# Kernel tuning notes

Hardware: AMD Instinct MI355X
Metric: run time of the kernel (lower is better)

## Reference

```python
import jax, jax.numpy as jnp
import numpy as np

D_INNER = 5120
DT_RANK = 160
N_STATE = 16
BATCH = 256


def _softplus_thresh20(x):
    # ttnn.softplus(parameter1=1.0, parameter2=20.0): linear above threshold 20
    return jnp.where(x > 20.0, x, jnp.log1p(jnp.exp(jnp.minimum(x, 20.0))))


def setup_inputs() -> dict:
    key = jax.random.key(0)
    ks = jax.random.split(key, 9)
    x = jax.random.normal(ks[0], (1, 1, BATCH, D_INNER), dtype=jnp.float32)
    # scale weights by 1/sqrt(fan_in) so softplus input is O(1)
    W_dt_low = jax.random.normal(ks[1], (D_INNER, DT_RANK), dtype=jnp.float32) / np.sqrt(D_INNER)
    W_dt = jax.random.normal(ks[2], (DT_RANK, D_INNER), dtype=jnp.float32) / np.sqrt(DT_RANK)
    b_dt = jax.random.normal(ks[3], (D_INNER,), dtype=jnp.float32)
    W_B = jax.random.normal(ks[4], (D_INNER, N_STATE), dtype=jnp.float32) / np.sqrt(D_INNER)
    W_C = jax.random.normal(ks[5], (D_INNER, N_STATE), dtype=jnp.float32) / np.sqrt(D_INNER)
    # A = -exp(A_log): strictly negative, as in the module's preprocess_A
    A = -jnp.exp(0.5 * jax.random.normal(ks[6], (D_INNER, N_STATE), dtype=jnp.float32))
    D = jax.random.normal(ks[7], (D_INNER,), dtype=jnp.float32)
    h0 = 0.1 * jax.random.normal(ks[8], (BATCH, D_INNER, N_STATE), dtype=jnp.float32)
    return {"x": x, "W_dt_low": W_dt_low, "W_dt": W_dt, "b_dt": b_dt,
            "W_B": W_B, "W_C": W_C, "A": A, "D": D, "h0": h0}


def reference(x, W_dt_low, W_dt, b_dt, W_B, W_C, A, D, h0):
    b, d = x.shape[2], x.shape[3]
    xb = x.reshape(b, d)                                  # (B, D)
    # delta = softplus(x @ x_proj_dt @ dt_proj + bias)
    delta = _softplus_thresh20(xb @ W_dt_low @ W_dt + b_dt)   # (B, D)
    Bp = xb @ W_B                                         # (B, N)
    Cp = xb @ W_C                                         # (B, N)
    # discretize: abar = exp(delta * A), bbar = delta * B
    # layout (B, D, N) matches repeat_interleave(delta, n) / repeat(B, d)
    abar = jnp.exp(delta[:, :, None] * A[None, :, :])     # (B, D, N)
    bbar = delta[:, :, None] * Bp[:, None, :]             # (B, D, N)
    h = abar * h0 + bbar * xb[:, :, None]                 # (B, D, N)
    y = jnp.einsum('bdn,bn->bd', h, Cp)                   # reduce over state
    out = xb * D[None, :] + y                             # (B, D)
    return out.reshape(1, 1, b, d)
```

## Files before the change

kernel.cpp:

```cpp
#include <hip/hip_runtime.h>
#include <math.h>

#define D_INNER 5120
#define DT_RANK 160
#define N_STATE 16
#define BATCH   256
#define KTOT    192

#define BGRP    8
#define NBG     (BATCH / BGRP)
#define DDBLK   160
#define NDDB    (D_INNER / DDBLK)
#define SPLIT   32

#define K3_BT   4

#define OFF_T     0
#define SZ_T      (BATCH * KTOT)
#define OFF_P     (OFF_T + SZ_T)
#define SZ_P      (SPLIT * BATCH * KTOT)
#define OFF_SBC   (OFF_P + SZ_P)

__global__ __launch_bounds__(256) void k1_gemm(const float* __restrict__ x,
                                               const float* __restrict__ Wdtlow,
                                               const float* __restrict__ WB,
                                               const float* __restrict__ WC,
                                               float* __restrict__ ws) {
    __shared__ float lds[4 * BGRP * KTOT];
    const int tid  = threadIdx.x;
    const int lane = tid & 63;
    const int wv   = tid >> 6;
    const int b0   = blockIdx.x * BGRP;
    const int ddB  = blockIdx.y * DDBLK;

    float* xs = lds;
    for (int j = tid; j < (BGRP * DDBLK) / 4; j += 256) {
        int i  = j / (DDBLK / 4);
        int c4 = j % (DDBLK / 4);
        float4 v = *(const float4*)(x + (size_t)(b0 + i) * D_INNER + ddB + c4 * 4);
        *(float4*)(xs + i * DDBLK + c4 * 4) = v;
    }
    __syncthreads();

    const int dd0 = wv * 40;
    const float* p0 = Wdtlow + (size_t)(ddB + dd0) * DT_RANK + lane;
    const float* p1 = p0 + 64;
    const float* p2;
    int st2;
    if (lane < 32)      { p2 = p0 + 128;                                          st2 = DT_RANK; }
    else if (lane < 48) { p2 = WB + (size_t)(ddB + dd0) * N_STATE + (lane - 32);  st2 = N_STATE; }
    else                { p2 = WC + (size_t)(ddB + dd0) * N_STATE + (lane - 48);  st2 = N_STATE; }

    float acc0[BGRP], acc1[BGRP], acc2[BGRP];
#pragma unroll
    for (int i = 0; i < BGRP; ++i) { acc0[i] = 0.f; acc1[i] = 0.f; acc2[i] = 0.f; }

#pragma unroll 2
    for (int g = 0; g < 10; ++g) {
        float w0[4], w1[4], w2[4];
#pragma unroll
        for (int u = 0; u < 4; ++u) {
            int dd = g * 4 + u;
            w0[u] = p0[(size_t)dd * DT_RANK];
            w1[u] = p1[(size_t)dd * DT_RANK];
            w2[u] = p2[(size_t)dd * st2];
        }
#pragma unroll
        for (int i = 0; i < BGRP; ++i) {
            float4 xv = *(const float4*)(xs + i * DDBLK + dd0 + g * 4);
            acc0[i] += xv.x * w0[0] + xv.y * w0[1] + xv.z * w0[2] + xv.w * w0[3];
            acc1[i] += xv.x * w1[0] + xv.y * w1[1] + xv.z * w1[2] + xv.w * w1[3];
            acc2[i] += xv.x * w2[0] + xv.y * w2[1] + xv.z * w2[2] + xv.w * w2[3];
        }
    }
    __syncthreads();

#pragma unroll
    for (int i = 0; i < BGRP; ++i) {
        float* r = lds + wv * (BGRP * KTOT) + i * KTOT;
        r[lane]       = acc0[i];
        r[lane + 64]  = acc1[i];
        r[lane + 128] = acc2[i];
    }
    __syncthreads();

    float* P = ws + OFF_P + (size_t)blockIdx.y * (BATCH * KTOT) + (size_t)b0 * KTOT;
#pragma unroll
    for (int r = 0; r < 6; ++r) {
        int idx = tid + r * 256;
        P[idx] = lds[idx] + lds[idx + 1536] + lds[idx + 3072] + lds[idx + 4608];
    }
}

__global__ __launch_bounds__(192) void k2_reduce(float* __restrict__ ws) {
    __shared__ float ts[KTOT];
    const int b   = blockIdx.x;
    const int col = threadIdx.x;
    const float* P = ws + OFF_P + (size_t)b * KTOT + col;
    float a = 0.f;
#pragma unroll
    for (int s = 0; s < SPLIT; ++s) a += P[(size_t)s * (BATCH * KTOT)];
    ws[OFF_T + b * KTOT + col] = a;
    ts[col] = a;
    __syncthreads();
    if (col == 0) {
        float s2 = 0.f;
#pragma unroll
        for (int n = 0; n < N_STATE; ++n) s2 += ts[160 + n] * ts[176 + n];
        ws[OFF_SBC + b] = s2;
    }
}

__global__ __launch_bounds__(256, 5) void k3_fused(const float* __restrict__ Wdt,
                                                   const float* __restrict__ b_dt,
                                                   const float* __restrict__ x,
                                                   const float* __restrict__ A,
                                                   const float* __restrict__ Dv,
                                                   const float* __restrict__ h0,
                                                   const float* __restrict__ ws,
                                                   float* __restrict__ out) {
    const int tid = threadIdx.x;
    const int d   = blockIdx.x * 256 + tid;
    const int b0  = blockIdx.y * K3_BT;
    const float* T  = ws + OFF_T;
    const float* SB = ws + OFF_SBC;

    const float4* hb = (const float4*)(h0 + ((size_t)b0 * D_INNER + d) * N_STATE);
    const size_t  hstride = (size_t)D_INNER * 4;

    float4 hc0 = hb[0], hc1 = hb[1], hc2 = hb[2], hc3 = hb[3];
    const float4* h1p = hb + hstride;
    float4 hn0 = h1p[0], hn1 = h1p[1], hn2 = h1p[2], hn3 = h1p[3];

    float xv[K3_BT];
#pragma unroll
    for (int i = 0; i < K3_BT; ++i) xv[i] = x[(size_t)(b0 + i) * D_INNER + d];

    const float bdt = b_dt[d];
    const float Dd  = Dv[d];
    const float4* a4 = (const float4*)(A + (size_t)d * N_STATE);
    float4 a0 = a4[0], a1 = a4[1], a2 = a4[2], a3 = a4[3];

    float acc[K3_BT] = {0.f, 0.f, 0.f, 0.f};
#pragma unroll 8
    for (int k = 0; k < DT_RANK; ++k) {
        float w = Wdt[(size_t)k * D_INNER + d];
#pragma unroll
        for (int i = 0; i < K3_BT; ++i)
            acc[i] += T[(size_t)(b0 + i) * KTOT + k] * w;
    }

#pragma unroll
    for (int i = 0; i < K3_BT; ++i) {
        float4 p0, p1, p2, p3;
        if (i + 2 < K3_BT) {
            const float4* hp = hb + (size_t)(i + 2) * hstride;
            p0 = hp[0]; p1 = hp[1]; p2 = hp[2]; p3 = hp[3];
        }

        const int b = b0 + i;
        const float* Tb = T + (size_t)b * KTOT;

        float v     = acc[i] + bdt;
        float delta = (v > 20.f) ? v : log1pf(__expf(v));
        float sbc   = SB[b];

        float y0, y1, y2, y3;
        y0  = __expf(delta * a0.x) * hc0.x * Tb[176 + 0];
        y0 += __expf(delta * a0.y) * hc0.y * Tb[176 + 1];
        y0 += __expf(delta * a0.z) * hc0.z * Tb[176 + 2];
        y0 += __expf(delta * a0.w) * hc0.w * Tb[176 + 3];
        y1  = __expf(delta * a1.x) * hc1.x * Tb[176 + 4];
        y1 += __expf(delta * a1.y) * hc1.y * Tb[176 + 5];
        y1 += __expf(delta * a1.z) * hc1.z * Tb[176 + 6];
        y1 += __expf(delta * a1.w) * hc1.w * Tb[176 + 7];
        y2  = __expf(delta * a2.x) * hc2.x * Tb[176 + 8];
        y2 += __expf(delta * a2.y) * hc2.y * Tb[176 + 9];
        y2 += __expf(delta * a2.z) * hc2.z * Tb[176 + 10];
        y2 += __expf(delta * a2.w) * hc2.w * Tb[176 + 11];
        y3  = __expf(delta * a3.x) * hc3.x * Tb[176 + 12];
        y3 += __expf(delta * a3.y) * hc3.y * Tb[176 + 13];
        y3 += __expf(delta * a3.z) * hc3.z * Tb[176 + 14];
        y3 += __expf(delta * a3.w) * hc3.w * Tb[176 + 15];

        out[(size_t)b * D_INNER + d] = xv[i] * (Dd + delta * sbc)
                                     + ((y0 + y1) + (y2 + y3));

        if (i < K3_BT - 1) { hc0 = hn0; hc1 = hn1; hc2 = hn2; hc3 = hn3; }
        if (i + 2 < K3_BT) { hn0 = p0;  hn1 = p1;  hn2 = p2;  hn3 = p3;  }
    }
}

extern "C" void kernel_launch(void* const* d_in, const int* in_sizes, int n_in,
                              void* d_out, int out_size, void* d_ws, size_t ws_size,
                              hipStream_t stream) {
    const float* x      = (const float*)d_in[0];
    const float* Wdtlow = (const float*)d_in[1];
    const float* Wdt    = (const float*)d_in[2];
    const float* bdt    = (const float*)d_in[3];
    const float* WB     = (const float*)d_in[4];
    const float* WC     = (const float*)d_in[5];
    const float* A      = (const float*)d_in[6];
    const float* Dv     = (const float*)d_in[7];
    const float* h0     = (const float*)d_in[8];
    float* ws  = (float*)d_ws;
    float* out = (float*)d_out;

    hipLaunchKernelGGL(k1_gemm, dim3(NBG, NDDB), dim3(256), 0, stream,
                       x, Wdtlow, WB, WC, ws);
    hipLaunchKernelGGL(k2_reduce, dim3(BATCH), dim3(192), 0, stream, ws);
    hipLaunchKernelGGL(k3_fused, dim3(D_INNER / 256, BATCH / K3_BT), dim3(256),
                       0, stream, Wdt, bdt, x, A, Dv, h0, ws, out);
}
```

Before: 173.1 us.

## Double-buffer Wdt chunks into LDS via async global_load_lds in k3

The dt_proj inner loop in k3_fused now stages Wdt in chunks of 16 rows into two LDS buffers using the async global-to-LDS load builtin. The next chunk is prefetched while the current one is consumed, and a barrier separates the chunks. The goal is to hide global-load latency for the weight stream and free vector registers from direct loads. In exchange it adds 32 KB of LDS per block, which may limit occupancy, plus a block barrier in every chunk.

```diff
diff --git a/kernel.cpp b/kernel.cpp
--- a/kernel.cpp
+++ b/kernel.cpp
@@ -14,6 +14,8 @@
 #define SPLIT   32
 
 #define K3_BT   4
+#define KC      16
+#define NCHUNK  (DT_RANK / KC)
 
 #define OFF_T     0
 #define SZ_T      (BATCH * KTOT)
@@ -119,9 +121,14 @@
                                                    const float* __restrict__ h0,
                                                    const float* __restrict__ ws,
                                                    float* __restrict__ out) {
-    const int tid = threadIdx.x;
-    const int d   = blockIdx.x * 256 + tid;
-    const int b0  = blockIdx.y * K3_BT;
+    __shared__ float ldsA[KC * 256];
+    __shared__ float ldsB[KC * 256];
+    const int tid  = threadIdx.x;
+    const int lane = tid & 63;
+    const int wv4  = (tid >> 6) * 4;
+    const int dblk = blockIdx.x * 256;
+    const int d    = dblk + tid;
+    const int b0   = blockIdx.y * K3_BT;
     const float* T  = ws + OFF_T;
     const float* SB = ws + OFF_SBC;
 
@@ -141,14 +148,49 @@
     const float4* a4 = (const float4*)(A + (size_t)d * N_STATE);
     float4 a0 = a4[0], a1 = a4[1], a2 = a4[2], a3 = a4[3];
 
-    float acc[K3_BT] = {0.f, 0.f, 0.f, 0.f};
-#pragma unroll 8
-    for (int k = 0; k < DT_RANK; ++k) {
-        float w = Wdt[(size_t)k * D_INNER + d];
-#pragma unroll
-        for (int i = 0; i < K3_BT; ++i)
-            acc[i] += T[(size_t)(b0 + i) * KTOT + k] * w;
-    }
+#define STAGE(KC0, DSTBUF)                                                    \
+    {                                                                         \
+        _Pragma("unroll")                                                     \
+        for (int u = 0; u < 4; ++u) {                                         \
+            const int r = wv4 + u;                                            \
+            const float* s = Wdt + (size_t)((KC0) + r) * D_INNER              \
+                           + dblk + lane * 4;                                 \
+            __builtin_amdgcn_global_load_lds(                                 \
+                (const __attribute__((address_space(1))) void*)s,             \
+                (__attribute__((address_space(3))) void*)((DSTBUF) + r * 256),\
+                16, 0, 0);                                                    \
+        }                                                                     \
+    }
+
+    const float* tA = T + (size_t)b0 * KTOT;
+    const float* tB = tA + KTOT;
+    const float* tC = tB + KTOT;
+    const float* tD = tC + KTOT;
+
+    float acc0 = 0.f, acc1 = 0.f, acc2 = 0.f, acc3 = 0.f;
+
+    STAGE(0, ldsA)
+    __syncthreads();
+
+#pragma unroll 1
+    for (int c = 0; c < NCHUNK; ++c) {
+        if (c < NCHUNK - 1) STAGE((c + 1) * KC, (c & 1) ? ldsA : ldsB)
+        const float* cb = (c & 1) ? ldsB : ldsA;
+        const int kbase = c * KC;
+#pragma unroll
+        for (int kk = 0; kk < KC; ++kk) {
+            float w = cb[kk * 256 + tid];
+            int   k = kbase + kk;
+            acc0 += tA[k] * w;
+            acc1 += tB[k] * w;
+            acc2 += tC[k] * w;
+            acc3 += tD[k] * w;
+        }
+        __syncthreads();
+    }
+#undef STAGE
+
+    float accv[K3_BT] = {acc0, acc1, acc2, acc3};
 
 #pragma unroll
     for (int i = 0; i < K3_BT; ++i) {
@@ -161,7 +203,7 @@
         const int b = b0 + i;
         const float* Tb = T + (size_t)b * KTOT;
 
-        float v     = acc[i] + bdt;
+        float v     = accv[i] + bdt;
         float delta = (v > 20.f) ? v : log1pf(__expf(v));
         float sbc   = SB[b];
 
```

New measurement: 175.7 us. No clear change (+1.5%).

## Split k3 across four lanes per channel with coalesced h0 loads and LDS-staged T

Applied to the files above, without the earlier changes.

Restructures the fused kernel so each channel d is handled by four lanes, each owning four of the sixteen states. Each lane also computes a quarter of the rank-160 dt projection, and the partial sums are combined with cross-lane shuffles. h0 and A are now read as fully contiguous float4 per thread, and the T rows are staged in LDS instead of being read through global memory. The aim is better coalescing of the dominant h0 stream and less per-thread register pressure (launch bounds raised to 6). The cost is four times the blocks, duplicate loads of x/b_dt/D across the four lanes, and extra shuffles.

```diff
diff --git a/kernel.cpp b/kernel.cpp
--- a/kernel.cpp
+++ b/kernel.cpp
@@ -14,6 +14,7 @@
 #define SPLIT   32
 
 #define K3_BT   4
+#define K3_DD   64
 
 #define OFF_T     0
 #define SZ_T      (BATCH * KTOT)
@@ -111,7 +112,7 @@
     }
 }
 
-__global__ __launch_bounds__(256, 5) void k3_fused(const float* __restrict__ Wdt,
+__global__ __launch_bounds__(256, 6) void k3_fused(const float* __restrict__ Wdt,
                                                    const float* __restrict__ b_dt,
                                                    const float* __restrict__ x,
                                                    const float* __restrict__ A,
@@ -119,75 +120,81 @@
                                                    const float* __restrict__ h0,
                                                    const float* __restrict__ ws,
                                                    float* __restrict__ out) {
-    const int tid = threadIdx.x;
-    const int d   = blockIdx.x * 256 + tid;
-    const int b0  = blockIdx.y * K3_BT;
-    const float* T  = ws + OFF_T;
+    __shared__ __align__(16) float Tl[K3_BT * KTOT];
+    const int tid  = threadIdx.x;
+    const int did  = tid >> 2;
+    const int ng   = tid & 3;
+    const int dblk = blockIdx.x * K3_DD;
+    const int d    = dblk + did;
+    const int b0   = blockIdx.y * K3_BT;
     const float* SB = ws + OFF_SBC;
 
-    const float4* hb = (const float4*)(h0 + ((size_t)b0 * D_INNER + d) * N_STATE);
-    const size_t  hstride = (size_t)D_INNER * 4;
-
-    float4 hc0 = hb[0], hc1 = hb[1], hc2 = hb[2], hc3 = hb[3];
-    const float4* h1p = hb + hstride;
-    float4 hn0 = h1p[0], hn1 = h1p[1], hn2 = h1p[2], hn3 = h1p[3];
+    {
+        const float* Tg = ws + OFF_T + (size_t)b0 * KTOT;
+#pragma unroll
+        for (int j = tid; j < K3_BT * KTOT; j += 256) Tl[j] = Tg[j];
+    }
+
+    float4 h[K3_BT];
+#pragma unroll
+    for (int bi = 0; bi < K3_BT; ++bi)
+        h[bi] = *(const float4*)(h0 + ((size_t)(b0 + bi) * D_INNER + dblk) * N_STATE
+                                 + tid * 4);
+    float4 av = *(const float4*)(A + (size_t)dblk * N_STATE + tid * 4);
 
     float xv[K3_BT];
 #pragma unroll
-    for (int i = 0; i < K3_BT; ++i) xv[i] = x[(size_t)(b0 + i) * D_INNER + d];
+    for (int bi = 0; bi < K3_BT; ++bi) xv[bi] = x[(size_t)(b0 + bi) * D_INNER + d];
 
     const float bdt = b_dt[d];
     const float Dd  = Dv[d];
-    const float4* a4 = (const float4*)(A + (size_t)d * N_STATE);
-    float4 a0 = a4[0], a1 = a4[1], a2 = a4[2], a3 = a4[3];
+
+    __syncthreads();
 
     float acc[K3_BT] = {0.f, 0.f, 0.f, 0.f};
-#pragma unroll 8
-    for (int k = 0; k < DT_RANK; ++k) {
-        float w = Wdt[(size_t)k * D_INNER + d];
-#pragma unroll
-        for (int i = 0; i < K3_BT; ++i)
-            acc[i] += T[(size_t)(b0 + i) * KTOT + k] * w;
-    }
-
-#pragma unroll
-    for (int i = 0; i < K3_BT; ++i) {
-        float4 p0, p1, p2, p3;
-        if (i + 2 < K3_BT) {
-            const float4* hp = hb + (size_t)(i + 2) * hstride;
-            p0 = hp[0]; p1 = hp[1]; p2 = hp[2]; p3 = hp[3];
+    {
+        const float* wp = Wdt + (size_t)(ng * 40) * D_INNER + d;
+        const int kb = ng * 40;
+#pragma unroll 2
+        for (int q = 0; q < 10; ++q) {
+            float w0 = wp[(size_t)(q * 4 + 0) * D_INNER];
+            float w1 = wp[(size_t)(q * 4 + 1) * D_INNER];
+            float w2 = wp[(size_t)(q * 4 + 2) * D_INNER];
+            float w3 = wp[(size_t)(q * 4 + 3) * D_INNER];
+#pragma unroll
+            for (int bi = 0; bi < K3_BT; ++bi) {
+                float4 t = *(const float4*)&Tl[bi * KTOT + kb + q * 4];
+                acc[bi] += t.x * w0;
+                acc[bi] += t.y * w1;
+                acc[bi] += t.z * w2;
+                acc[bi] += t.w * w3;
+            }
         }
-
-        const int b = b0 + i;
-        const float* Tb = T + (size_t)b * KTOT;
-
-        float v     = acc[i] + bdt;
+    }
+#pragma unroll
+    for (int bi = 0; bi < K3_BT; ++bi) {
+        acc[bi] += __shfl_xor(acc[bi], 1);
+        acc[bi] += __shfl_xor(acc[bi], 2);
+    }
+
+#pragma unroll
+    for (int bi = 0; bi < K3_BT; ++bi) {
+        const int b = b0 + bi;
+        float v     = acc[bi] + bdt;
         float delta = (v > 20.f) ? v : log1pf(__expf(v));
         float sbc   = SB[b];
 
-        float y0, y1, y2, y3;
-        y0  = __expf(delta * a0.x) * hc0.x * Tb[176 + 0];
-        y0 += __expf(delta * a0.y) * hc0.y * Tb[176 + 1];
-        y0 += __expf(delta * a0.z) * hc0.z * Tb[176 + 2];
-        y0 += __expf(delta * a0.w) * hc0.w * Tb[176 + 3];
-        y1  = __expf(delta * a1.x) * hc1.x * Tb[176 + 4];
-        y1 += __expf(delta * a1.y) * hc1.y * Tb[176 + 5];
-        y1 += __expf(delta * a1.z) * hc1.z * Tb[176 + 6];
-        y1 += __expf(delta * a1.w) * hc1.w * Tb[176 + 7];
-        y2  = __expf(delta * a2.x) * hc2.x * Tb[176 + 8];
-        y2 += __expf(delta * a2.y) * hc2.y * Tb[176 + 9];
-        y2 += __expf(delta * a2.z) * hc2.z * Tb[176 + 10];
-        y2 += __expf(delta * a2.w) * hc2.w * Tb[176 + 11];
-        y3  = __expf(delta * a3.x) * hc3.x * Tb[176 + 12];
-        y3 += __expf(delta * a3.y) * hc3.y * Tb[176 + 13];
-        y3 += __expf(delta * a3.z) * hc3.z * Tb[176 + 14];
-        y3 += __expf(delta * a3.w) * hc3.w * Tb[176 + 15];
-
-        out[(size_t)b * D_INNER + d] = xv[i] * (Dd + delta * sbc)
-                                     + ((y0 + y1) + (y2 + y3));
-
-        if (i < K3_BT - 1) { hc0 = hn0; hc1 = hn1; hc2 = hn2; hc3 = hn3; }
-        if (i + 2 < K3_BT) { hn0 = p0;  hn1 = p1;  hn2 = p2;  hn3 = p3;  }
+        const float* Cb = &Tl[bi * KTOT + 176 + ng * 4];
+        float y;
+        y  = __expf(delta * av.x) * h[bi].x * Cb[0];
+        y += __expf(delta * av.y) * h[bi].y * Cb[1];
+        y += __expf(delta * av.z) * h[bi].z * Cb[2];
+        y += __expf(delta * av.w) * h[bi].w * Cb[3];
+        y += __shfl_xor(y, 1);
+        y += __shfl_xor(y, 2);
+
+        if (ng == bi)
+            out[(size_t)b * D_INNER + d] = xv[bi] * (Dd + delta * sbc) + y;
     }
 }
 
@@ -209,6 +216,6 @@
     hipLaunchKernelGGL(k1_gemm, dim3(NBG, NDDB), dim3(256), 0, stream,
                        x, Wdtlow, WB, WC, ws);
     hipLaunchKernelGGL(k2_reduce, dim3(BATCH), dim3(192), 0, stream, ws);
-    hipLaunchKernelGGL(k3_fused, dim3(D_INNER / 256, BATCH / K3_BT), dim3(256),
+    hipLaunchKernelGGL(k3_fused, dim3(D_INNER / K3_DD, BATCH / K3_BT), dim3(256),
                        0, stream, Wdt, bdt, x, A, Dv, h0, ws, out);
 }
```

New measurement: 187.0 us. 8.0% more time.

## Stage h0 tiles into LDS via async global_load_lds before the dt GEMV

Applied to the files above, without the earlier changes.

The k3 kernel now issues asynchronous global-to-LDS loads for all four batch rows of h0 at kernel start, then overlaps them with the dt projection loop. After a barrier each thread reads its 16 state values from LDS, replacing the register double-buffered prefetch. The aim is coalesced wide h0 traffic with lower register pressure. In exchange each block uses 64KB of LDS, which limits occupancy, and the min-blocks launch bound is dropped.

```diff
diff --git a/kernel.cpp b/kernel.cpp
--- a/kernel.cpp
+++ b/kernel.cpp
@@ -111,26 +111,37 @@
     }
 }
 
-__global__ __launch_bounds__(256, 5) void k3_fused(const float* __restrict__ Wdt,
-                                                   const float* __restrict__ b_dt,
-                                                   const float* __restrict__ x,
-                                                   const float* __restrict__ A,
-                                                   const float* __restrict__ Dv,
-                                                   const float* __restrict__ h0,
-                                                   const float* __restrict__ ws,
-                                                   float* __restrict__ out) {
-    const int tid = threadIdx.x;
-    const int d   = blockIdx.x * 256 + tid;
-    const int b0  = blockIdx.y * K3_BT;
+__global__ __launch_bounds__(256) void k3_fused(const float* __restrict__ Wdt,
+                                                const float* __restrict__ b_dt,
+                                                const float* __restrict__ x,
+                                                const float* __restrict__ A,
+                                                const float* __restrict__ Dv,
+                                                const float* __restrict__ h0,
+                                                const float* __restrict__ ws,
+                                                float* __restrict__ out) {
+    __shared__ __align__(16) float ldsH[K3_BT * 256 * N_STATE];
+    const int tid  = threadIdx.x;
+    const int lane = tid & 63;
+    const int wv   = tid >> 6;
+    const int dblk = blockIdx.x * 256;
+    const int d    = dblk + tid;
+    const int b0   = blockIdx.y * K3_BT;
     const float* T  = ws + OFF_T;
     const float* SB = ws + OFF_SBC;
 
-    const float4* hb = (const float4*)(h0 + ((size_t)b0 * D_INNER + d) * N_STATE);
-    const size_t  hstride = (size_t)D_INNER * 4;
-
-    float4 hc0 = hb[0], hc1 = hb[1], hc2 = hb[2], hc3 = hb[3];
-    const float4* h1p = hb + hstride;
-    float4 hn0 = h1p[0], hn1 = h1p[1], hn2 = h1p[2], hn3 = h1p[3];
+#pragma unroll
+    for (int b = 0; b < K3_BT; ++b) {
+#pragma unroll
+        for (int j = 0; j < 4; ++j) {
+            const float* s = h0 + ((size_t)(b0 + b) * D_INNER + dblk) * N_STATE
+                           + wv * 1024 + j * 256 + lane * 4;
+            float* dst = ldsH + b * 4096 + wv * 1024 + j * 256;
+            __builtin_amdgcn_global_load_lds(
+                (const __attribute__((address_space(1))) void*)s,
+                (__attribute__((address_space(3))) void*)dst,
+                16, 0, 0);
+        }
+    }
 
     float xv[K3_BT];
 #pragma unroll
@@ -141,25 +152,31 @@
     const float4* a4 = (const float4*)(A + (size_t)d * N_STATE);
     float4 a0 = a4[0], a1 = a4[1], a2 = a4[2], a3 = a4[3];
 
+    const float* tA = T + (size_t)b0 * KTOT;
+    const float* tB = tA + KTOT;
+    const float* tC = tB + KTOT;
+    const float* tD = tC + KTOT;
     float acc[K3_BT] = {0.f, 0.f, 0.f, 0.f};
 #pragma unroll 8
     for (int k = 0; k < DT_RANK; ++k) {
         float w = Wdt[(size_t)k * D_INNER + d];
-#pragma unroll
-        for (int i = 0; i < K3_BT; ++i)
-            acc[i] += T[(size_t)(b0 + i) * KTOT + k] * w;
-    }
+        acc[0] += tA[k] * w;
+        acc[1] += tB[k] * w;
+        acc[2] += tC[k] * w;
+        acc[3] += tD[k] * w;
+    }
+
+    __syncthreads();
 
 #pragma unroll
     for (int i = 0; i < K3_BT; ++i) {
-        float4 p0, p1, p2, p3;
-        if (i + 2 < K3_BT) {
-            const float4* hp = hb + (size_t)(i + 2) * hstride;
-            p0 = hp[0]; p1 = hp[1]; p2 = hp[2]; p3 = hp[3];
-        }
-
         const int b = b0 + i;
         const float* Tb = T + (size_t)b * KTOT;
+        const float* hl = ldsH + i * 4096 + tid * 16;
+        float4 hc0 = *(const float4*)(hl + 0);
+        float4 hc1 = *(const float4*)(hl + 4);
+        float4 hc2 = *(const float4*)(hl + 8);
+        float4 hc3 = *(const float4*)(hl + 12);
 
         float v     = acc[i] + bdt;
         float delta = (v > 20.f) ? v : log1pf(__expf(v));
@@ -185,9 +202,6 @@
 
         out[(size_t)b * D_INNER + d] = xv[i] * (Dd + delta * sbc)
                                      + ((y0 + y1) + (y2 + y3));
-
-        if (i < K3_BT - 1) { hc0 = hn0; hc1 = hn1; hc2 = hn2; hc3 = hn3; }
-        if (i + 2 < K3_BT) { hn0 = p0;  hn1 = p1;  hn2 = p2;  hn3 = p3;  }
     }
 }
 
```

After: 195.2 us. 12.8% more time.
